# Performance work log

Measured on AMD Instinct MI355X. Metric: run time of the kernel, lower is better.

## Reference

```python
import jax, jax.numpy as jnp
import numpy as np

HEADS = 8
DIM_HEAD = 64
QUERY_DIM = 512
INNER = HEADS * DIM_HEAD
T = 16
MAX_REL = 16  # == temporal_length
SCALE = DIM_HEAD ** -0.5


def _rel_idx(length_q, length_k):
    rq = jnp.arange(length_q)
    rk = jnp.arange(length_k)
    dist = rk[None, :] - rq[:, None]
    return jnp.clip(dist, -MAX_REL, MAX_REL) + MAX_REL  # [Tq, Tk] in [0, 2*MAX_REL]


def setup_inputs() -> dict:
    key = jax.random.key(0)
    ks = jax.random.split(key, 8)
    B = 2048
    s = 0.02
    return {
        "x": jax.random.normal(ks[0], (B, T, QUERY_DIM), dtype=jnp.float32),
        "Wq": jax.random.normal(ks[1], (QUERY_DIM, INNER), dtype=jnp.float32) * s,
        "Wk": jax.random.normal(ks[2], (QUERY_DIM, INNER), dtype=jnp.float32) * s,
        "Wv": jax.random.normal(ks[3], (QUERY_DIM, INNER), dtype=jnp.float32) * s,
        "Wo": jax.random.normal(ks[4], (INNER, QUERY_DIM), dtype=jnp.float32) * s,
        "bo": jnp.zeros((QUERY_DIM,), dtype=jnp.float32),
        "rel_k_table": jax.random.normal(ks[5], (2 * MAX_REL + 1, DIM_HEAD), dtype=jnp.float32) * s,
        "rel_v_table": jax.random.normal(ks[6], (2 * MAX_REL + 1, DIM_HEAD), dtype=jnp.float32) * s,
    }


def reference(x, Wq, Wk, Wv, Wo, bo, rel_k_table, rel_v_table):
    B, N, _ = x.shape
    # projections (Linear without bias)
    def split_heads(t):
        return t.reshape(B, N, HEADS, DIM_HEAD).transpose(0, 2, 1, 3)  # [B, H, N, D]
    q = split_heads(x @ Wq)
    k = split_heads(x @ Wk)
    v = split_heads(x @ Wv)

    sim = jnp.einsum('bhid,bhjd->bhij', q, k) * SCALE
    idx = _rel_idx(N, N)                     # [N, N]
    k2 = rel_k_table[idx]                    # [N, N, D]
    sim = sim + jnp.einsum('bhtd,tsd->bhts', q, k2) * SCALE

    attn = jax.nn.softmax(sim, axis=-1)
    out = jnp.einsum('bhij,bhjd->bhid', attn, v)
    v2 = rel_v_table[idx]                    # [N, N, D]
    out = out + jnp.einsum('bhts,tsd->bhtd', attn, v2)

    out = out.transpose(0, 2, 1, 3).reshape(B, N, INNER)
    return out @ Wo + bo
```

## Files before the change

### kernel.cpp

```cpp
#include <hip/hip_runtime.h>
#include <stdint.h>


using bf16x8 = __attribute__((ext_vector_type(8))) short;
using f32x4  = __attribute__((ext_vector_type(4))) float;

#define AS3P(p) ((__attribute__((address_space(3))) void*)(p))
#define AS1P(p) ((const __attribute__((address_space(1))) void*)(p))

__device__ __forceinline__ uint16_t f2bf(float f) {
  unsigned int x = __builtin_bit_cast(unsigned int, f);
  x += 0x7fffu + ((x >> 16) & 1u);
  return (uint16_t)(x >> 16);
}

__global__ void cast_kernel(const float* __restrict__ in, uint16_t* __restrict__ out, int n8) {
  int i = blockIdx.x * 256 + threadIdx.x;
  if (i >= n8) return;
  float4 a = ((const float4*)in)[i * 2];
  float4 b = ((const float4*)in)[i * 2 + 1];
  uint4 r;
  r.x = (uint32_t)f2bf(a.x) | ((uint32_t)f2bf(a.y) << 16);
  r.y = (uint32_t)f2bf(a.z) | ((uint32_t)f2bf(a.w) << 16);
  r.z = (uint32_t)f2bf(b.x) | ((uint32_t)f2bf(b.y) << 16);
  r.w = (uint32_t)f2bf(b.z) | ((uint32_t)f2bf(b.w) << 16);
  ((uint4*)out)[i] = r;
}

__global__ void transpose_cast4(const float* __restrict__ Wq, const float* __restrict__ Wk,
                                const float* __restrict__ Wv, const float* __restrict__ Wo,
                                uint16_t* __restrict__ WqkvT, uint16_t* __restrict__ WoT) {
  __shared__ float tile[32][33];
  const int z = blockIdx.z;
  const float* src = (z == 0) ? Wq : (z == 1) ? Wk : (z == 2) ? Wv : Wo;
  uint16_t* dst = (z == 3) ? WoT : (WqkvT + z * 262144);
  int tx = threadIdx.x, ty = threadIdx.y;
  int c0 = blockIdx.x * 32, r0 = blockIdx.y * 32;
  #pragma unroll
  for (int k = 0; k < 4; ++k)
    tile[ty + 8 * k][tx] = src[(r0 + ty + 8 * k) * 512 + c0 + tx];
  __syncthreads();
  #pragma unroll
  for (int k = 0; k < 4; ++k)
    dst[(c0 + ty + 8 * k) * 512 + r0 + tx] = f2bf(tile[tx][ty + 8 * k]);
}

template<int OUT_BF16, int KDIM>
__global__ __launch_bounds__(512, 2) void gemm256(
    const uint16_t* __restrict__ A, const uint16_t* __restrict__ B,
    void* __restrict__ C, const float* __restrict__ bias, int N, int nbx) {
  constexpr int NT = KDIM / 32;
  __shared__ __align__(16) uint16_t lds[4][2][8192];
  __shared__ __align__(16) uint16_t ldsO[8][1024];
  const int tid = threadIdx.x;
  const int w = tid >> 6, l = tid & 63;
  const int lr = l & 15, kc = l >> 4;
  const int wm = w >> 2, wn = w & 3;
  const int cpx = gridDim.x >> 3;
  const int id = blockIdx.x;
  const int swz = (id & 7) * cpx + (id >> 3);
  const int by = swz / nbx, bx = swz - by * nbx;
  const int mBase = by * 256, nBase = bx * 256;
  const int g8 = l >> 3;
  const int sub = (l & 7) ^ g8;
  const int srow = w * 32 + g8 * 2 + (sub >> 2);
  const int scol = (sub & 3) * 8;
  const uint16_t* gA0 = A + (size_t)(mBase + srow) * KDIM + scol;
  const uint16_t* gA1 = gA0 + 16 * KDIM;
  const uint16_t* gB0 = B + (size_t)(nBase + srow) * KDIM + scol;
  const uint16_t* gB1 = gB0 + 16 * KDIM;
  int offA[8], offB[4];
  #pragma unroll
  for (int m = 0; m < 8; ++m) {
    int row = wm * 128 + m * 16 + lr;
    int rp = row >> 1, sb = ((row & 1) << 2) | kc;
    offA[m] = rp * 128 + ((sb ^ (rp & 7)) << 4);
  }
  #pragma unroll
  for (int n = 0; n < 4; ++n) {
    int row = wn * 64 + n * 16 + lr;
    int rp = row >> 1, sb = ((row & 1) << 2) | kc;
    offB[n] = rp * 128 + ((sb ^ (rp & 7)) << 4);
  }
  f32x4 acc[8][4] = {};
  #pragma unroll
  for (int pt = 0; pt < 3; ++pt) {
    uint16_t* dA = &lds[pt][0][w * 1024];
    uint16_t* dB = &lds[pt][1][w * 1024];
    __builtin_amdgcn_global_load_lds(AS1P(gA0 + pt * 32), AS3P(dA),       16, 0, 0);
    __builtin_amdgcn_global_load_lds(AS1P(gA1 + pt * 32), AS3P(dA + 512), 16, 0, 0);
    __builtin_amdgcn_global_load_lds(AS1P(gB0 + pt * 32), AS3P(dB),       16, 0, 0);
    __builtin_amdgcn_global_load_lds(AS1P(gB1 + pt * 32), AS3P(dB + 512), 16, 0, 0);
  }
  asm volatile("s_waitcnt vmcnt(8)" ::: "memory");
  __builtin_amdgcn_s_barrier();
  #pragma unroll 4
  for (int t = 0; t < NT; ++t) {
    const int bi = t & 3;
    const int si = (t + 3) & 3;
    const char* bufA = (const char*)&lds[bi][0][0];
    const char* bufB = (const char*)&lds[bi][1][0];
    if (t + 3 < NT) {
      uint16_t* dA = &lds[si][0][w * 1024];
      __builtin_amdgcn_global_load_lds(AS1P(gA0 + (t + 3) * 32), AS3P(dA),       16, 0, 0);
      __builtin_amdgcn_global_load_lds(AS1P(gA1 + (t + 3) * 32), AS3P(dA + 512), 16, 0, 0);
    }
    if (t + 3 < NT)       asm volatile("s_waitcnt vmcnt(6)" ::: "memory");
    else if (t + 3 == NT) asm volatile("s_waitcnt vmcnt(4)" ::: "memory");
    else if (t + 2 == NT) asm volatile("s_waitcnt vmcnt(0)" ::: "memory");
    bf16x8 a0 = *(const bf16x8*)(bufA + offA[0]);
    bf16x8 a1 = *(const bf16x8*)(bufA + offA[1]);
    bf16x8 a2 = *(const bf16x8*)(bufA + offA[2]);
    bf16x8 a3 = *(const bf16x8*)(bufA + offA[3]);
    bf16x8 b0 = *(const bf16x8*)(bufB + offB[0]);
    bf16x8 b1 = *(const bf16x8*)(bufB + offB[1]);
    bf16x8 b2 = *(const bf16x8*)(bufB + offB[2]);
    bf16x8 b3 = *(const bf16x8*)(bufB + offB[3]);
    __builtin_amdgcn_sched_barrier(0);
    __builtin_amdgcn_s_barrier();
    asm volatile("s_waitcnt lgkmcnt(0)" ::: "memory");
    __builtin_amdgcn_sched_barrier(0);
    __builtin_amdgcn_s_setprio(1);
    acc[0][0] = __builtin_amdgcn_mfma_f32_16x16x32_bf16(a0, b0, acc[0][0], 0, 0, 0);
    acc[0][1] = __builtin_amdgcn_mfma_f32_16x16x32_bf16(a0, b1, acc[0][1], 0, 0, 0);
    acc[0][2] = __builtin_amdgcn_mfma_f32_16x16x32_bf16(a0, b2, acc[0][2], 0, 0, 0);
    acc[0][3] = __builtin_amdgcn_mfma_f32_16x16x32_bf16(a0, b3, acc[0][3], 0, 0, 0);
    acc[1][0] = __builtin_amdgcn_mfma_f32_16x16x32_bf16(a1, b0, acc[1][0], 0, 0, 0);
    acc[1][1] = __builtin_amdgcn_mfma_f32_16x16x32_bf16(a1, b1, acc[1][1], 0, 0, 0);
    acc[1][2] = __builtin_amdgcn_mfma_f32_16x16x32_bf16(a1, b2, acc[1][2], 0, 0, 0);
    acc[1][3] = __builtin_amdgcn_mfma_f32_16x16x32_bf16(a1, b3, acc[1][3], 0, 0, 0);
    acc[2][0] = __builtin_amdgcn_mfma_f32_16x16x32_bf16(a2, b0, acc[2][0], 0, 0, 0);
    acc[2][1] = __builtin_amdgcn_mfma_f32_16x16x32_bf16(a2, b1, acc[2][1], 0, 0, 0);
    acc[2][2] = __builtin_amdgcn_mfma_f32_16x16x32_bf16(a2, b2, acc[2][2], 0, 0, 0);
    acc[2][3] = __builtin_amdgcn_mfma_f32_16x16x32_bf16(a2, b3, acc[2][3], 0, 0, 0);
    acc[3][0] = __builtin_amdgcn_mfma_f32_16x16x32_bf16(a3, b0, acc[3][0], 0, 0, 0);
    acc[3][1] = __builtin_amdgcn_mfma_f32_16x16x32_bf16(a3, b1, acc[3][1], 0, 0, 0);
    acc[3][2] = __builtin_amdgcn_mfma_f32_16x16x32_bf16(a3, b2, acc[3][2], 0, 0, 0);
    acc[3][3] = __builtin_amdgcn_mfma_f32_16x16x32_bf16(a3, b3, acc[3][3], 0, 0, 0);
    __builtin_amdgcn_s_setprio(0);
    __builtin_amdgcn_sched_barrier(0);
    __builtin_amdgcn_s_barrier();
    if (t + 3 < NT) {
      uint16_t* dB = &lds[si][1][w * 1024];
      __builtin_amdgcn_global_load_lds(AS1P(gB0 + (t + 3) * 32), AS3P(dB),       16, 0, 0);
      __builtin_amdgcn_global_load_lds(AS1P(gB1 + (t + 3) * 32), AS3P(dB + 512), 16, 0, 0);
    }
    bf16x8 a4 = *(const bf16x8*)(bufA + offA[4]);
    bf16x8 a5 = *(const bf16x8*)(bufA + offA[5]);
    bf16x8 a6 = *(const bf16x8*)(bufA + offA[6]);
    bf16x8 a7 = *(const bf16x8*)(bufA + offA[7]);
    __builtin_amdgcn_sched_barrier(0);
    __builtin_amdgcn_s_barrier();
    asm volatile("s_waitcnt lgkmcnt(0)" ::: "memory");
    __builtin_amdgcn_sched_barrier(0);
    __builtin_amdgcn_s_setprio(1);
    acc[4][0] = __builtin_amdgcn_mfma_f32_16x16x32_bf16(a4, b0, acc[4][0], 0, 0, 0);
    acc[4][1] = __builtin_amdgcn_mfma_f32_16x16x32_bf16(a4, b1, acc[4][1], 0, 0, 0);
    acc[4][2] = __builtin_amdgcn_mfma_f32_16x16x32_bf16(a4, b2, acc[4][2], 0, 0, 0);
    acc[4][3] = __builtin_amdgcn_mfma_f32_16x16x32_bf16(a4, b3, acc[4][3], 0, 0, 0);
    acc[5][0] = __builtin_amdgcn_mfma_f32_16x16x32_bf16(a5, b0, acc[5][0], 0, 0, 0);
    acc[5][1] = __builtin_amdgcn_mfma_f32_16x16x32_bf16(a5, b1, acc[5][1], 0, 0, 0);
    acc[5][2] = __builtin_amdgcn_mfma_f32_16x16x32_bf16(a5, b2, acc[5][2], 0, 0, 0);
    acc[5][3] = __builtin_amdgcn_mfma_f32_16x16x32_bf16(a5, b3, acc[5][3], 0, 0, 0);
    acc[6][0] = __builtin_amdgcn_mfma_f32_16x16x32_bf16(a6, b0, acc[6][0], 0, 0, 0);
    acc[6][1] = __builtin_amdgcn_mfma_f32_16x16x32_bf16(a6, b1, acc[6][1], 0, 0, 0);
    acc[6][2] = __builtin_amdgcn_mfma_f32_16x16x32_bf16(a6, b2, acc[6][2], 0, 0, 0);
    acc[6][3] = __builtin_amdgcn_mfma_f32_16x16x32_bf16(a6, b3, acc[6][3], 0, 0, 0);
    acc[7][0] = __builtin_amdgcn_mfma_f32_16x16x32_bf16(a7, b0, acc[7][0], 0, 0, 0);
    acc[7][1] = __builtin_amdgcn_mfma_f32_16x16x32_bf16(a7, b1, acc[7][1], 0, 0, 0);
    acc[7][2] = __builtin_amdgcn_mfma_f32_16x16x32_bf16(a7, b2, acc[7][2], 0, 0, 0);
    acc[7][3] = __builtin_amdgcn_mfma_f32_16x16x32_bf16(a7, b3, acc[7][3], 0, 0, 0);
    __builtin_amdgcn_s_setprio(0);
    __builtin_amdgcn_sched_barrier(0);
    __builtin_amdgcn_s_barrier();
  }
  if (OUT_BF16) {
    uint16_t* oW = &ldsO[w][0];
    const int t2 = l >> 3, c2 = l & 7;
    uint16_t* gO = (uint16_t*)C + (size_t)(mBase + wm * 128 + t2) * N + (nBase + wn * 64 + c2 * 8);
    #pragma unroll
    for (int m = 0; m < 8; ++m) {
      #pragma unroll
      for (int n = 0; n < 4; ++n)
        #pragma unroll
        for (int r = 0; r < 4; ++r) {
          const int tt = kc * 4 + r;
          const int d = n * 16 + lr;
          const int col = (((d >> 3) ^ (tt & 7)) << 3) | (d & 7);
          oW[tt * 64 + col] = f2bf(acc[m][n][r]);
        }
      asm volatile("s_waitcnt lgkmcnt(0)" ::: "memory");
      __builtin_amdgcn_sched_barrier(0);
      bf16x8 s0 = *(const bf16x8*)(oW + t2 * 64 + (((c2 ^ (t2 & 7)) << 3)));
      bf16x8 s1 = *(const bf16x8*)(oW + (8 + t2) * 64 + (((c2 ^ (t2 & 7)) << 3)));
      *(bf16x8*)(gO + (size_t)(m * 16) * N) = s0;
      *(bf16x8*)(gO + (size_t)(m * 16 + 8) * N) = s1;
      asm volatile("s_waitcnt lgkmcnt(0)" ::: "memory");
      __builtin_amdgcn_sched_barrier(0);
    }
  } else {
    #pragma unroll
    for (int m = 0; m < 8; ++m)
      #pragma unroll
      for (int n = 0; n < 4; ++n) {
        const int col = nBase + wn * 64 + n * 16 + lr;
        #pragma unroll
        for (int r = 0; r < 4; ++r) {
          const int row = mBase + wm * 128 + m * 16 + kc * 4 + r;
          ((float*)C)[(size_t)row * N + col] = acc[m][n][r] + bias[col];
        }
      }
  }
}

__global__ __launch_bounds__(512) void attn_kernel(
    const uint16_t* __restrict__ qkv,
    const float* __restrict__ relk, const float* __restrict__ relv,
    uint16_t* __restrict__ outA) {
  __shared__ __align__(16) uint16_t relkS[33 * 72];
  __shared__ __align__(16) uint16_t relvT[64 * 40];
  __shared__ __align__(16) uint16_t vT[8][64 * 24];
  __shared__ float attnS[8][16 * 17];
  const int tid = threadIdx.x;
  for (int e = tid; e < 33 * 64; e += 512) {
    int j = e >> 6, d = e & 63;
    relkS[j * 72 + d] = f2bf(relk[e]);
    relvT[d * 40 + j] = f2bf(relv[e]);
  }
  const int w = tid >> 6, l = tid & 63;
  const int bh = blockIdx.x * 8 + w;
  const int b = bh >> 3, h = bh & 7;
  const int rowBase = b * 16;
  const int lr = l & 15, kc = l >> 4;
  const uint16_t* qrow = qkv + (size_t)(rowBase + lr) * 1536 + h * 64;
  bf16x8 aq0 = *(const bf16x8*)(qrow + kc * 8);
  bf16x8 aq1 = *(const bf16x8*)(qrow + 32 + kc * 8);
  const uint16_t* krow = qrow + 512;
  bf16x8 bk0 = *(const bf16x8*)(krow + kc * 8);
  bf16x8 bk1 = *(const bf16x8*)(krow + 32 + kc * 8);
  {
    const int s = l >> 2, dg = l & 3;
    const uint16_t* vrow = qkv + (size_t)(rowBase + s) * 1536 + 1024 + h * 64 + dg * 16;
    uint4 v0 = *(const uint4*)vrow;
    uint4 v1 = *(const uint4*)(vrow + 8);
    uint16_t tmp[16];
    *(uint4*)(tmp) = v0; *(uint4*)(tmp + 8) = v1;
    #pragma unroll
    for (int i = 0; i < 16; ++i)
      vT[w][(dg * 16 + i) * 24 + s] = tmp[i];
  }
  __syncthreads();
  const f32x4 zero = {0.f, 0.f, 0.f, 0.f};
  f32x4 sim = __builtin_amdgcn_mfma_f32_16x16x32_bf16(aq0, bk0, zero, 0, 0, 0);
  sim = __builtin_amdgcn_mfma_f32_16x16x32_bf16(aq1, bk1, sim, 0, 0, 0);
  bf16x8 rka0 = *(const bf16x8*)(relkS + lr * 72 + kc * 8);
  bf16x8 rka1 = *(const bf16x8*)(relkS + lr * 72 + 32 + kc * 8);
  bf16x8 rkb0 = *(const bf16x8*)(relkS + (16 + lr) * 72 + kc * 8);
  bf16x8 rkb1 = *(const bf16x8*)(relkS + (16 + lr) * 72 + 32 + kc * 8);
  f32x4 rqa = __builtin_amdgcn_mfma_f32_16x16x32_bf16(aq0, rka0, zero, 0, 0, 0);
  rqa = __builtin_amdgcn_mfma_f32_16x16x32_bf16(aq1, rka1, rqa, 0, 0, 0);
  f32x4 rqb = __builtin_amdgcn_mfma_f32_16x16x32_bf16(aq0, rkb0, zero, 0, 0, 0);
  rqb = __builtin_amdgcn_mfma_f32_16x16x32_bf16(aq1, rkb1, rqb, 0, 0, 0);
  #pragma unroll
  for (int r = 0; r < 4; ++r) {
    const int t = kc * 4 + r;
    const int j = lr - t + 16;
    const int src = (l & 48) | (j & 15);
    const float va = __shfl(rqa[r], src, 64);
    const float vb = __shfl(rqb[r], src, 64);
    const float rqv = (j < 16) ? va : vb;
    float sv = (sim[r] + rqv) * 0.125f;
    float m = sv;
    m = fmaxf(m, __shfl_xor(m, 1, 64));
    m = fmaxf(m, __shfl_xor(m, 2, 64));
    m = fmaxf(m, __shfl_xor(m, 4, 64));
    m = fmaxf(m, __shfl_xor(m, 8, 64));
    const float p = __expf(sv - m);
    float su = p;
    su += __shfl_xor(su, 1, 64);
    su += __shfl_xor(su, 2, 64);
    su += __shfl_xor(su, 4, 64);
    su += __shfl_xor(su, 8, 64);
    attnS[w][t * 17 + lr] = p / su;
  }
  __syncthreads();
  const float* aS = attnS[w];
  bf16x8 attnA, w2A;
  #pragma unroll
  for (int i = 0; i < 8; ++i) {
    const int s1 = kc * 8 + i;
    attnA[i] = (s1 < 16) ? (short)f2bf(aS[lr * 17 + s1]) : (short)0;
    const int s2 = s1 + lr - 16;
    w2A[i] = (s2 >= 0 && s2 < 16) ? (short)f2bf(aS[lr * 17 + s2]) : (short)0;
  }
  f32x4 o[4];
  #pragma unroll
  for (int dt = 0; dt < 4; ++dt) {
    bf16x8 vf  = *(const bf16x8*)(&vT[w][(dt * 16 + lr) * 24 + (kc & 1) * 8]);
    bf16x8 rvf = *(const bf16x8*)(&relvT[(dt * 16 + lr) * 40 + kc * 8]);
    o[dt] = __builtin_amdgcn_mfma_f32_16x16x32_bf16(w2A, rvf, zero, 0, 0, 0);
    o[dt] = __builtin_amdgcn_mfma_f32_16x16x32_bf16(attnA, vf, o[dt], 0, 0, 0);
  }
  asm volatile("s_waitcnt lgkmcnt(0)" ::: "memory");
  __builtin_amdgcn_sched_barrier(0);
  uint16_t* oW = &vT[w][0];
  #pragma unroll
  for (int dt = 0; dt < 4; ++dt)
    #pragma unroll
    for (int r = 0; r < 4; ++r) {
      const int t = kc * 4 + r;
      const int chunk = dt * 2 + (lr >> 3);
      oW[t * 64 + ((chunk ^ (t & 7)) << 3) + (lr & 7)] = f2bf(o[dt][r]);
    }
  asm volatile("s_waitcnt lgkmcnt(0)" ::: "memory");
  __builtin_amdgcn_sched_barrier(0);
  const int t2 = l >> 3, c2 = l & 7;
  bf16x8 s0 = *(const bf16x8*)(oW + t2 * 64 + ((c2 ^ (t2 & 7)) << 3));
  bf16x8 s1 = *(const bf16x8*)(oW + (8 + t2) * 64 + ((c2 ^ (t2 & 7)) << 3));
  *(bf16x8*)(outA + (size_t)(rowBase + t2) * 512 + h * 64 + c2 * 8) = s0;
  *(bf16x8*)(outA + (size_t)(rowBase + 8 + t2) * 512 + h * 64 + c2 * 8) = s1;
}

extern "C" void kernel_launch(void* const* d_in, const int* in_sizes, int n_in,
                              void* d_out, int out_size, void* d_ws, size_t ws_size,
                              hipStream_t stream) {
  const float* x    = (const float*)d_in[0];
  const float* Wq   = (const float*)d_in[1];
  const float* Wk   = (const float*)d_in[2];
  const float* Wv   = (const float*)d_in[3];
  const float* Wo   = (const float*)d_in[4];
  const float* bo   = (const float*)d_in[5];
  const float* relk = (const float*)d_in[6];
  const float* relv = (const float*)d_in[7];

  char* ws = (char*)d_ws;
  uint16_t* qkv   = (uint16_t*)ws;
  uint16_t* xbf   = (uint16_t*)(ws + 100663296);
  uint16_t* WqkvT = (uint16_t*)(ws + 134217728);
  uint16_t* WoT   = (uint16_t*)(ws + 135790592);
  uint16_t* attnO = xbf;

  cast_kernel<<<8192, 256, 0, stream>>>(x, xbf, 2097152);
  transpose_cast4<<<dim3(16, 16, 4), dim3(32, 8), 0, stream>>>(Wq, Wk, Wv, Wo, WqkvT, WoT);
  gemm256<1, 512><<<dim3(768), dim3(512), 0, stream>>>(xbf, WqkvT, (void*)qkv, nullptr, 1536, 6);
  attn_kernel<<<2048, 512, 0, stream>>>(qkv, relk, relv, attnO);
  gemm256<0, 512><<<dim3(256), dim3(512), 0, stream>>>(attnO, WoT, d_out, bo, 512, 2);
}
```

Before: 141.9 us.

## Fuse QKV projection GEMM with relative-position attention in one kernel

Replaces the separate QKV GEMM and attention kernel with a single kernel. Each block computes a 256x192 tile of head-interleaved Q/K/V for one head and 16 batches, stages it in LDS, and runs the attention directly. The weight transpose is changed to interleave Q, K and V columns per head so one tile covers a full head. This removes the round trip of the large qkv intermediate through global memory and one launch, at the cost of a large LDS footprint, likely lower occupancy, and a narrower N tile.

```diff
diff --git a/kernel.cpp b/kernel.cpp
--- a/kernel.cpp
+++ b/kernel.cpp
@@ -33,7 +33,6 @@
   __shared__ float tile[32][33];
   const int z = blockIdx.z;
   const float* src = (z == 0) ? Wq : (z == 1) ? Wk : (z == 2) ? Wv : Wo;
-  uint16_t* dst = (z == 3) ? WoT : (WqkvT + z * 262144);
   int tx = threadIdx.x, ty = threadIdx.y;
   int c0 = blockIdx.x * 32, r0 = blockIdx.y * 32;
   #pragma unroll
@@ -41,8 +40,236 @@
     tile[ty + 8 * k][tx] = src[(r0 + ty + 8 * k) * 512 + c0 + tx];
   __syncthreads();
   #pragma unroll
-  for (int k = 0; k < 4; ++k)
-    dst[(c0 + ty + 8 * k) * 512 + r0 + tx] = f2bf(tile[tx][ty + 8 * k]);
+  for (int k = 0; k < 4; ++k) {
+    const int n = c0 + ty + 8 * k;
+    uint16_t v = f2bf(tile[tx][ty + 8 * k]);
+    if (z == 3) WoT[(size_t)n * 512 + r0 + tx] = v;
+    else {
+      const int np = (n >> 6) * 192 + z * 64 + (n & 63);
+      WqkvT[(size_t)np * 512 + r0 + tx] = v;
+    }
+  }
+}
+
+template<int KDIM>
+__global__ __launch_bounds__(512, 2) void gemm_attn(
+    const uint16_t* __restrict__ A, const uint16_t* __restrict__ B,
+    const float* __restrict__ relk, const float* __restrict__ relv,
+    uint16_t* __restrict__ outA) {
+  constexpr int NT = KDIM / 64;
+  __shared__ __align__(16) char smem[149760];
+  uint16_t* ldsA = (uint16_t*)smem;
+  uint16_t* ldsB = (uint16_t*)(smem + 98304);
+  const int tid = threadIdx.x;
+  const int w = tid >> 6, l = tid & 63;
+  const int lr = l & 15, kc = l >> 4;
+  const int wm = w >> 2, wn = w & 3;
+  const int cpx = gridDim.x >> 3;
+  const int id = blockIdx.x;
+  const int swz = (id & 7) * cpx + (id >> 3);
+  const int by = swz >> 3, bx = swz & 7;
+  const int mBase = by * 256, nBase = bx * 192;
+  const int g8 = l >> 3;
+  const int cs = ((l & 7) ^ g8) * 8;
+  const uint16_t* gA = A + (size_t)(mBase + w * 32 + g8) * KDIM + cs;
+  const uint16_t* gB = B + (size_t)(nBase + w * 24 + g8) * KDIM + cs;
+  int offA[8], offB[3];
+  #pragma unroll
+  for (int m = 0; m < 8; ++m) {
+    int row = wm * 128 + m * 16 + lr;
+    offA[m] = row * 128 + ((kc ^ (row & 7)) << 4);
+  }
+  #pragma unroll
+  for (int n = 0; n < 3; ++n) {
+    int row = wn * 48 + n * 16 + lr;
+    offB[n] = row * 128 + ((kc ^ (row & 7)) << 4);
+  }
+  f32x4 acc[8][3] = {};
+
+#define STAGE_A(t, bf) do { \
+    uint16_t* d = ldsA + (bf) * 16384 + w * 2048; \
+    const uint16_t* s = gA + (t) * 64; \
+    __builtin_amdgcn_global_load_lds(AS1P(s),              AS3P(d),        16, 0, 0); \
+    __builtin_amdgcn_global_load_lds(AS1P(s + 8  * KDIM),  AS3P(d + 512),  16, 0, 0); \
+    __builtin_amdgcn_global_load_lds(AS1P(s + 16 * KDIM),  AS3P(d + 1024), 16, 0, 0); \
+    __builtin_amdgcn_global_load_lds(AS1P(s + 24 * KDIM),  AS3P(d + 1536), 16, 0, 0); \
+  } while (0)
+#define STAGE_B(t, bf) do { \
+    uint16_t* d = ldsB + (bf) * 12288 + w * 1536; \
+    const uint16_t* s = gB + (t) * 64; \
+    __builtin_amdgcn_global_load_lds(AS1P(s),              AS3P(d),        16, 0, 0); \
+    __builtin_amdgcn_global_load_lds(AS1P(s + 8  * KDIM),  AS3P(d + 512),  16, 0, 0); \
+    __builtin_amdgcn_global_load_lds(AS1P(s + 16 * KDIM),  AS3P(d + 1024), 16, 0, 0); \
+  } while (0)
+
+  STAGE_A(0, 0); STAGE_B(0, 0); STAGE_A(1, 1);
+  asm volatile("s_waitcnt vmcnt(4)" ::: "memory");
+  __builtin_amdgcn_s_barrier();
+
+  #pragma unroll
+  for (int t = 0; t < NT; ++t) {
+    const int ba = t % 3, bb2 = t & 1;
+    const char* bufA = (const char*)(ldsA + ba * 16384);
+    const char* bufB = (const char*)(ldsB + bb2 * 12288);
+    if (t + 1 < NT) STAGE_B(t + 1, (t + 1) & 1);
+    if (t + 2 < NT) STAGE_A(t + 2, (t + 2) % 3);
+    bf16x8 a0[8], b0[3];
+    #pragma unroll
+    for (int m = 0; m < 8; ++m) a0[m] = *(const bf16x8*)(bufA + offA[m]);
+    #pragma unroll
+    for (int n = 0; n < 3; ++n) b0[n] = *(const bf16x8*)(bufB + offB[n]);
+    __builtin_amdgcn_sched_barrier(0);
+    __builtin_amdgcn_s_barrier();
+    asm volatile("s_waitcnt lgkmcnt(0)" ::: "memory");
+    __builtin_amdgcn_sched_barrier(0);
+    __builtin_amdgcn_s_setprio(1);
+    #pragma unroll
+    for (int m = 0; m < 8; ++m)
+      #pragma unroll
+      for (int n = 0; n < 3; ++n)
+        acc[m][n] = __builtin_amdgcn_mfma_f32_16x16x32_bf16(a0[m], b0[n], acc[m][n], 0, 0, 0);
+    __builtin_amdgcn_s_setprio(0);
+    __builtin_amdgcn_sched_barrier(0);
+    __builtin_amdgcn_s_barrier();
+    bf16x8 a1[8], b1[3];
+    #pragma unroll
+    for (int m = 0; m < 8; ++m) a1[m] = *(const bf16x8*)(bufA + (offA[m] ^ 64));
+    #pragma unroll
+    for (int n = 0; n < 3; ++n) b1[n] = *(const bf16x8*)(bufB + (offB[n] ^ 64));
+    if (t < NT - 2) asm volatile("s_waitcnt vmcnt(4)" ::: "memory");
+    else            asm volatile("s_waitcnt vmcnt(0)" ::: "memory");
+    __builtin_amdgcn_sched_barrier(0);
+    __builtin_amdgcn_s_barrier();
+    asm volatile("s_waitcnt lgkmcnt(0)" ::: "memory");
+    __builtin_amdgcn_sched_barrier(0);
+    __builtin_amdgcn_s_setprio(1);
+    #pragma unroll
+    for (int m = 0; m < 8; ++m)
+      #pragma unroll
+      for (int n = 0; n < 3; ++n)
+        acc[m][n] = __builtin_amdgcn_mfma_f32_16x16x32_bf16(a1[m], b1[n], acc[m][n], 0, 0, 0);
+    __builtin_amdgcn_s_setprio(0);
+    __builtin_amdgcn_sched_barrier(0);
+    __builtin_amdgcn_s_barrier();
+  }
+#undef STAGE_A
+#undef STAGE_B
+
+  __syncthreads();
+  uint16_t* Qs    = (uint16_t*)smem;
+  uint16_t* Ks    = (uint16_t*)(smem + 32768);
+  uint16_t* Vs    = (uint16_t*)(smem + 65536);
+  uint16_t* relkS = (uint16_t*)(smem + 114688);
+  uint16_t* relvT = (uint16_t*)(smem + 119552);
+  float*    attnS = (float*)(smem + 124672);
+  uint16_t* oWall = (uint16_t*)(smem + 133376);
+  for (int e = tid; e < 33 * 64; e += 512) {
+    int j = e >> 6, d = e & 63;
+    relkS[j * 72 + d] = f2bf(relk[e]);
+    relvT[d * 40 + j] = f2bf(relv[e]);
+  }
+  #pragma unroll
+  for (int m = 0; m < 8; ++m) {
+    const int b = wm * 8 + m;
+    #pragma unroll
+    for (int n = 0; n < 3; ++n) {
+      const int g = wn * 3 + n;
+      const int arr = g >> 2;
+      const int db = ((g & 3) << 4) + lr;
+      #pragma unroll
+      for (int r = 0; r < 4; ++r) {
+        const int tt = kc * 4 + r;
+        const uint16_t val = f2bf(acc[m][n][r]);
+        if (arr == 0)      Qs[b * 1024 + tt * 64 + db] = val;
+        else if (arr == 1) Ks[b * 1024 + tt * 64 + db] = val;
+        else               Vs[b * 1536 + db * 24 + tt] = val;
+      }
+    }
+  }
+  __syncthreads();
+  const f32x4 zero = {0.f, 0.f, 0.f, 0.f};
+  float* aSb = attnS + w * 272;
+  uint16_t* oW = oWall + w * 1024;
+  bf16x8 rka0 = *(const bf16x8*)(relkS + lr * 72 + kc * 8);
+  bf16x8 rka1 = *(const bf16x8*)(relkS + lr * 72 + 32 + kc * 8);
+  bf16x8 rkb0 = *(const bf16x8*)(relkS + (16 + lr) * 72 + kc * 8);
+  bf16x8 rkb1 = *(const bf16x8*)(relkS + (16 + lr) * 72 + 32 + kc * 8);
+  #pragma unroll
+  for (int bb = 0; bb < 2; ++bb) {
+    const int b = w * 2 + bb;
+    const uint16_t* Qb = Qs + b * 1024;
+    const uint16_t* Kb = Ks + b * 1024;
+    const uint16_t* Vb = Vs + b * 1536;
+    bf16x8 aq0 = *(const bf16x8*)(Qb + lr * 64 + kc * 8);
+    bf16x8 aq1 = *(const bf16x8*)(Qb + lr * 64 + 32 + kc * 8);
+    bf16x8 bk0 = *(const bf16x8*)(Kb + lr * 64 + kc * 8);
+    bf16x8 bk1 = *(const bf16x8*)(Kb + lr * 64 + 32 + kc * 8);
+    f32x4 sim = __builtin_amdgcn_mfma_f32_16x16x32_bf16(aq0, bk0, zero, 0, 0, 0);
+    sim = __builtin_amdgcn_mfma_f32_16x16x32_bf16(aq1, bk1, sim, 0, 0, 0);
+    f32x4 rqa = __builtin_amdgcn_mfma_f32_16x16x32_bf16(aq0, rka0, zero, 0, 0, 0);
+    rqa = __builtin_amdgcn_mfma_f32_16x16x32_bf16(aq1, rka1, rqa, 0, 0, 0);
+    f32x4 rqb = __builtin_amdgcn_mfma_f32_16x16x32_bf16(aq0, rkb0, zero, 0, 0, 0);
+    rqb = __builtin_amdgcn_mfma_f32_16x16x32_bf16(aq1, rkb1, rqb, 0, 0, 0);
+    #pragma unroll
+    for (int r = 0; r < 4; ++r) {
+      const int t = kc * 4 + r;
+      const int j = lr - t + 16;
+      const int src = (l & 48) | (j & 15);
+      const float va = __shfl(rqa[r], src, 64);
+      const float vb = __shfl(rqb[r], src, 64);
+      const float rqv = (j < 16) ? va : vb;
+      float sv = (sim[r] + rqv) * 0.125f;
+      float m = sv;
+      m = fmaxf(m, __shfl_xor(m, 1, 64));
+      m = fmaxf(m, __shfl_xor(m, 2, 64));
+      m = fmaxf(m, __shfl_xor(m, 4, 64));
+      m = fmaxf(m, __shfl_xor(m, 8, 64));
+      const float p = __expf(sv - m);
+      float su = p;
+      su += __shfl_xor(su, 1, 64);
+      su += __shfl_xor(su, 2, 64);
+      su += __shfl_xor(su, 4, 64);
+      su += __shfl_xor(su, 8, 64);
+      aSb[t * 17 + lr] = p / su;
+    }
+    asm volatile("s_waitcnt lgkmcnt(0)" ::: "memory");
+    __builtin_amdgcn_sched_barrier(0);
+    bf16x8 attnA, w2A;
+    #pragma unroll
+    for (int i = 0; i < 8; ++i) {
+      const int s1 = kc * 8 + i;
+      attnA[i] = (s1 < 16) ? (short)f2bf(aSb[lr * 17 + s1]) : (short)0;
+      const int s2 = s1 + lr - 16;
+      w2A[i] = (s2 >= 0 && s2 < 16) ? (short)f2bf(aSb[lr * 17 + s2]) : (short)0;
+    }
+    f32x4 o[4];
+    #pragma unroll
+    for (int dt = 0; dt < 4; ++dt) {
+      bf16x8 vf  = *(const bf16x8*)(Vb + (dt * 16 + lr) * 24 + (kc & 1) * 8);
+      bf16x8 rvf = *(const bf16x8*)(relvT + (dt * 16 + lr) * 40 + kc * 8);
+      o[dt] = __builtin_amdgcn_mfma_f32_16x16x32_bf16(w2A, rvf, zero, 0, 0, 0);
+      o[dt] = __builtin_amdgcn_mfma_f32_16x16x32_bf16(attnA, vf, o[dt], 0, 0, 0);
+    }
+    asm volatile("s_waitcnt lgkmcnt(0)" ::: "memory");
+    __builtin_amdgcn_sched_barrier(0);
+    #pragma unroll
+    for (int dt = 0; dt < 4; ++dt)
+      #pragma unroll
+      for (int r = 0; r < 4; ++r) {
+        const int t = kc * 4 + r;
+        const int chunk = dt * 2 + (lr >> 3);
+        oW[t * 64 + ((chunk ^ (t & 7)) << 3) + (lr & 7)] = f2bf(o[dt][r]);
+      }
+    asm volatile("s_waitcnt lgkmcnt(0)" ::: "memory");
+    __builtin_amdgcn_sched_barrier(0);
+    const int t2 = l >> 3, c2 = l & 7;
+    bf16x8 s0 = *(const bf16x8*)(oW + t2 * 64 + ((c2 ^ (t2 & 7)) << 3));
+    bf16x8 s1 = *(const bf16x8*)(oW + (8 + t2) * 64 + ((c2 ^ (t2 & 7)) << 3));
+    asm volatile("s_waitcnt lgkmcnt(0)" ::: "memory");
+    __builtin_amdgcn_sched_barrier(0);
+    *(bf16x8*)(outA + (size_t)(mBase + b * 16 + t2) * 512 + bx * 64 + c2 * 8) = s0;
+    *(bf16x8*)(outA + (size_t)(mBase + b * 16 + 8 + t2) * 512 + bx * 64 + c2 * 8) = s1;
+  }
 }
 
 template<int OUT_BF16, int KDIM>
@@ -51,7 +278,6 @@
     void* __restrict__ C, const float* __restrict__ bias, int N, int nbx) {
   constexpr int NT = KDIM / 32;
   __shared__ __align__(16) uint16_t lds[4][2][8192];
-  __shared__ __align__(16) uint16_t ldsO[8][1024];
   const int tid = threadIdx.x;
   const int w = tid >> 6, l = tid & 63;
   const int lr = l & 15, kc = l >> 4;
@@ -174,151 +400,18 @@
     __builtin_amdgcn_sched_barrier(0);
     __builtin_amdgcn_s_barrier();
   }
-  if (OUT_BF16) {
-    uint16_t* oW = &ldsO[w][0];
-    const int t2 = l >> 3, c2 = l & 7;
-    uint16_t* gO = (uint16_t*)C + (size_t)(mBase + wm * 128 + t2) * N + (nBase + wn * 64 + c2 * 8);
-    #pragma unroll
-    for (int m = 0; m < 8; ++m) {
+  #pragma unroll
+  for (int m = 0; m < 8; ++m)
+    #pragma unroll
+    for (int n = 0; n < 4; ++n) {
+      const int col = nBase + wn * 64 + n * 16 + lr;
       #pragma unroll
-      for (int n = 0; n < 4; ++n)
-        #pragma unroll
-        for (int r = 0; r < 4; ++r) {
-          const int tt = kc * 4 + r;
-          const int d = n * 16 + lr;
-          const int col = (((d >> 3) ^ (tt & 7)) << 3) | (d & 7);
-          oW[tt * 64 + col] = f2bf(acc[m][n][r]);
-        }
-      asm volatile("s_waitcnt lgkmcnt(0)" ::: "memory");
-      __builtin_amdgcn_sched_barrier(0);
-      bf16x8 s0 = *(const bf16x8*)(oW + t2 * 64 + (((c2 ^ (t2 & 7)) << 3)));
-      bf16x8 s1 = *(const bf16x8*)(oW + (8 + t2) * 64 + (((c2 ^ (t2 & 7)) << 3)));
-      *(bf16x8*)(gO + (size_t)(m * 16) * N) = s0;
-      *(bf16x8*)(gO + (size_t)(m * 16 + 8) * N) = s1;
-      asm volatile("s_waitcnt lgkmcnt(0)" ::: "memory");
-      __builtin_amdgcn_sched_barrier(0);
-    }
-  } else {
-    #pragma unroll
-    for (int m = 0; m < 8; ++m)
-      #pragma unroll
-      for (int n = 0; n < 4; ++n) {
-        const int col = nBase + wn * 64 + n * 16 + lr;
-        #pragma unroll
-        for (int r = 0; r < 4; ++r) {
-          const int row = mBase + wm * 128 + m * 16 + kc * 4 + r;
-          ((float*)C)[(size_t)row * N + col] = acc[m][n][r] + bias[col];
-        }
+      for (int r = 0; r < 4; ++r) {
+        const int row = mBase + wm * 128 + m * 16 + kc * 4 + r;
+        if (OUT_BF16) ((uint16_t*)C)[(size_t)row * N + col] = f2bf(acc[m][n][r]);
+        else          ((float*)C)[(size_t)row * N + col]    = acc[m][n][r] + bias[col];
       }
-  }
-}
-
-__global__ __launch_bounds__(512) void attn_kernel(
-    const uint16_t* __restrict__ qkv,
-    const float* __restrict__ relk, const float* __restrict__ relv,
-    uint16_t* __restrict__ outA) {
-  __shared__ __align__(16) uint16_t relkS[33 * 72];
-  __shared__ __align__(16) uint16_t relvT[64 * 40];
-  __shared__ __align__(16) uint16_t vT[8][64 * 24];
-  __shared__ float attnS[8][16 * 17];
-  const int tid = threadIdx.x;
-  for (int e = tid; e < 33 * 64; e += 512) {
-    int j = e >> 6, d = e & 63;
-    relkS[j * 72 + d] = f2bf(relk[e]);
-    relvT[d * 40 + j] = f2bf(relv[e]);
-  }
-  const int w = tid >> 6, l = tid & 63;
-  const int bh = blockIdx.x * 8 + w;
-  const int b = bh >> 3, h = bh & 7;
-  const int rowBase = b * 16;
-  const int lr = l & 15, kc = l >> 4;
-  const uint16_t* qrow = qkv + (size_t)(rowBase + lr) * 1536 + h * 64;
-  bf16x8 aq0 = *(const bf16x8*)(qrow + kc * 8);
-  bf16x8 aq1 = *(const bf16x8*)(qrow + 32 + kc * 8);
-  const uint16_t* krow = qrow + 512;
-  bf16x8 bk0 = *(const bf16x8*)(krow + kc * 8);
-  bf16x8 bk1 = *(const bf16x8*)(krow + 32 + kc * 8);
-  {
-    const int s = l >> 2, dg = l & 3;
-    const uint16_t* vrow = qkv + (size_t)(rowBase + s) * 1536 + 1024 + h * 64 + dg * 16;
-    uint4 v0 = *(const uint4*)vrow;
-    uint4 v1 = *(const uint4*)(vrow + 8);
-    uint16_t tmp[16];
-    *(uint4*)(tmp) = v0; *(uint4*)(tmp + 8) = v1;
-    #pragma unroll
-    for (int i = 0; i < 16; ++i)
-      vT[w][(dg * 16 + i) * 24 + s] = tmp[i];
-  }
-  __syncthreads();
-  const f32x4 zero = {0.f, 0.f, 0.f, 0.f};
-  f32x4 sim = __builtin_amdgcn_mfma_f32_16x16x32_bf16(aq0, bk0, zero, 0, 0, 0);
-  sim = __builtin_amdgcn_mfma_f32_16x16x32_bf16(aq1, bk1, sim, 0, 0, 0);
-  bf16x8 rka0 = *(const bf16x8*)(relkS + lr * 72 + kc * 8);
-  bf16x8 rka1 = *(const bf16x8*)(relkS + lr * 72 + 32 + kc * 8);
-  bf16x8 rkb0 = *(const bf16x8*)(relkS + (16 + lr) * 72 + kc * 8);
-  bf16x8 rkb1 = *(const bf16x8*)(relkS + (16 + lr) * 72 + 32 + kc * 8);
-  f32x4 rqa = __builtin_amdgcn_mfma_f32_16x16x32_bf16(aq0, rka0, zero, 0, 0, 0);
-  rqa = __builtin_amdgcn_mfma_f32_16x16x32_bf16(aq1, rka1, rqa, 0, 0, 0);
-  f32x4 rqb = __builtin_amdgcn_mfma_f32_16x16x32_bf16(aq0, rkb0, zero, 0, 0, 0);
-  rqb = __builtin_amdgcn_mfma_f32_16x16x32_bf16(aq1, rkb1, rqb, 0, 0, 0);
-  #pragma unroll
-  for (int r = 0; r < 4; ++r) {
-    const int t = kc * 4 + r;
-    const int j = lr - t + 16;
-    const int src = (l & 48) | (j & 15);
-    const float va = __shfl(rqa[r], src, 64);
-    const float vb = __shfl(rqb[r], src, 64);
-    const float rqv = (j < 16) ? va : vb;
-    float sv = (sim[r] + rqv) * 0.125f;
-    float m = sv;
-    m = fmaxf(m, __shfl_xor(m, 1, 64));
-    m = fmaxf(m, __shfl_xor(m, 2, 64));
-    m = fmaxf(m, __shfl_xor(m, 4, 64));
-    m = fmaxf(m, __shfl_xor(m, 8, 64));
-    const float p = __expf(sv - m);
-    float su = p;
-    su += __shfl_xor(su, 1, 64);
-    su += __shfl_xor(su, 2, 64);
-    su += __shfl_xor(su, 4, 64);
-    su += __shfl_xor(su, 8, 64);
-    attnS[w][t * 17 + lr] = p / su;
-  }
-  __syncthreads();
-  const float* aS = attnS[w];
-  bf16x8 attnA, w2A;
-  #pragma unroll
-  for (int i = 0; i < 8; ++i) {
-    const int s1 = kc * 8 + i;
-    attnA[i] = (s1 < 16) ? (short)f2bf(aS[lr * 17 + s1]) : (short)0;
-    const int s2 = s1 + lr - 16;
-    w2A[i] = (s2 >= 0 && s2 < 16) ? (short)f2bf(aS[lr * 17 + s2]) : (short)0;
-  }
-  f32x4 o[4];
-  #pragma unroll
-  for (int dt = 0; dt < 4; ++dt) {
-    bf16x8 vf  = *(const bf16x8*)(&vT[w][(dt * 16 + lr) * 24 + (kc & 1) * 8]);
-    bf16x8 rvf = *(const bf16x8*)(&relvT[(dt * 16 + lr) * 40 + kc * 8]);
-    o[dt] = __builtin_amdgcn_mfma_f32_16x16x32_bf16(w2A, rvf, zero, 0, 0, 0);
-    o[dt] = __builtin_amdgcn_mfma_f32_16x16x32_bf16(attnA, vf, o[dt], 0, 0, 0);
-  }
-  asm volatile("s_waitcnt lgkmcnt(0)" ::: "memory");
-  __builtin_amdgcn_sched_barrier(0);
-  uint16_t* oW = &vT[w][0];
-  #pragma unroll
-  for (int dt = 0; dt < 4; ++dt)
-    #pragma unroll
-    for (int r = 0; r < 4; ++r) {
-      const int t = kc * 4 + r;
-      const int chunk = dt * 2 + (lr >> 3);
-      oW[t * 64 + ((chunk ^ (t & 7)) << 3) + (lr & 7)] = f2bf(o[dt][r]);
-    }
-  asm volatile("s_waitcnt lgkmcnt(0)" ::: "memory");
-  __builtin_amdgcn_sched_barrier(0);
-  const int t2 = l >> 3, c2 = l & 7;
-  bf16x8 s0 = *(const bf16x8*)(oW + t2 * 64 + ((c2 ^ (t2 & 7)) << 3));
-  bf16x8 s1 = *(const bf16x8*)(oW + (8 + t2) * 64 + ((c2 ^ (t2 & 7)) << 3));
-  *(bf16x8*)(outA + (size_t)(rowBase + t2) * 512 + h * 64 + c2 * 8) = s0;
-  *(bf16x8*)(outA + (size_t)(rowBase + 8 + t2) * 512 + h * 64 + c2 * 8) = s1;
+    }
 }
 
 extern "C" void kernel_launch(void* const* d_in, const int* in_sizes, int n_in,
@@ -334,15 +427,13 @@
   const float* relv = (const float*)d_in[7];
 
   char* ws = (char*)d_ws;
-  uint16_t* qkv   = (uint16_t*)ws;
+  uint16_t* attnO = (uint16_t*)ws;
   uint16_t* xbf   = (uint16_t*)(ws + 100663296);
   uint16_t* WqkvT = (uint16_t*)(ws + 134217728);
   uint16_t* WoT   = (uint16_t*)(ws + 135790592);
-  uint16_t* attnO = xbf;
 
   cast_kernel<<<8192, 256, 0, stream>>>(x, xbf, 2097152);
   transpose_cast4<<<dim3(16, 16, 4), dim3(32, 8), 0, stream>>>(Wq, Wk, Wv, Wo, WqkvT, WoT);
-  gemm256<1, 512><<<dim3(768), dim3(512), 0, stream>>>(xbf, WqkvT, (void*)qkv, nullptr, 1536, 6);
-  attn_kernel<<<2048, 512, 0, stream>>>(qkv, relk, relv, attnO);
+  gemm_attn<512><<<dim3(1024), dim3(512), 0, stream>>>(xbf, WqkvT, relk, relv, attnO);
   gemm256<0, 512><<<dim3(256), dim3(512), 0, stream>>>(attnO, WoT, d_out, bo, 512, 2);
 }
```

Result: no change. 141.4 us (-0.4%).
